# Optimization experiments

Measured on AMD Instinct MI355X. Metric: run time of the kernel, lower is better.

The kernel has to match this reference:

```python
import jax, jax.numpy as jnp
import numpy as np

B, DIM, H, W, NH, WS = 128, 768, 16, 16, 12, 16
N = H * W  # 256, equals window_size**2


def setup_inputs() -> dict:
    key = jax.random.key(0)
    ks = jax.random.split(key, 8)
    s = 0.02  # small init scale for params
    return {
        "x": jax.random.normal(ks[0], (B, DIM, H, W), dtype=jnp.float32),
        "face_priors": jax.random.uniform(ks[1], (B, N, N), dtype=jnp.float32),
        "qkv_w": jax.random.normal(ks[2], (3 * DIM, DIM), dtype=jnp.float32) * s,
        "qkv_b": jax.random.normal(ks[3], (3 * DIM,), dtype=jnp.float32) * s,
        "rel_table": jax.random.normal(ks[4], ((2 * WS - 1) * (2 * WS - 1), NH), dtype=jnp.float32) * s,
        "face_prior": jax.random.normal(ks[5], (1, NH, N, N), dtype=jnp.float32) * s,
        "proj_w": jax.random.normal(ks[6], (DIM, DIM), dtype=jnp.float32) * s,
        "proj_b": jax.random.normal(ks[7], (DIM,), dtype=jnp.float32) * s,
    }


def _relative_position_bias(rel_table, h, w):
    # Static index computation (h, w are Python ints under jit).
    coords = jnp.stack(jnp.meshgrid(jnp.arange(h), jnp.arange(w), indexing="ij"))  # [2,h,w]
    flat = coords.reshape(2, -1)                     # [2, N]
    rel = flat[:, :, None] - flat[:, None, :]        # [2, N, N]
    idx = (rel[0] + h - 1) * (2 * w - 1) + (rel[1] + w - 1)  # [N, N]
    return rel_table[idx].transpose(2, 0, 1)         # [nh, N, N]


def reference(x, face_priors, qkv_w, qkv_b, rel_table, face_prior, proj_w, proj_b):
    b, c, h, w = x.shape
    n = h * w
    nh = face_prior.shape[1]
    hd = c // nh
    scale = hd ** -0.5

    x_flat = x.reshape(b, c, n).transpose(0, 2, 1)   # [B, N, C]
    qkv = (x_flat @ qkv_w.T + qkv_b).reshape(b, n, 3, nh, hd).transpose(2, 0, 3, 1, 4)
    q, k, v = qkv[0], qkv[1], qkv[2]                 # each [B, nh, N, hd]

    attn = jnp.einsum("bhnd,bhmd->bhnm", q, k) * scale
    attn = attn + face_prior + _relative_position_bias(rel_table, h, w)[None]
    attn = attn * face_priors[:, None]               # broadcast over heads
    attn = jax.nn.softmax(attn, axis=-1)

    out = jnp.einsum("bhnm,bhmd->bhnd", attn, v)     # [B, nh, N, hd]
    out = out.transpose(0, 2, 1, 3).reshape(b, n, c)
    out = out @ proj_w.T + proj_b                    # [B, N, C]
    return out.transpose(0, 2, 1).reshape(b, c, h, w)
```

## Files before the change

### kernel.cpp

```cpp
#include <hip/hip_runtime.h>

#define B_   128
#define DIM_ 768
#define NH_  12
#define HD_  64
#define N_   256

using half8 = __attribute__((ext_vector_type(8))) _Float16;
using half4 = __attribute__((ext_vector_type(4))) _Float16;
using f32x4 = __attribute__((ext_vector_type(4))) float;
typedef unsigned short u16;
typedef unsigned int   u32;


#define GLDS16(srcp, dstp) \
    __builtin_amdgcn_global_load_lds( \
        (const __attribute__((address_space(1))) void*)(srcp), \
        (__attribute__((address_space(3))) void*)(dstp), 16, 0, 0)

__device__ __forceinline__ int xcd_chunked(int orig, int nwg) {
    int xcd = orig & 7, loc = orig >> 3;
    int qq = nwg >> 3, rr = nwg & 7;
    return (xcd < rr ? xcd * (qq + 1) : rr * (qq + 1) + (xcd - rr) * qq) + loc;
}

__global__ __launch_bounds__(256) void bias16_kernel(
    const float* __restrict__ face_prior, const float* __restrict__ rel_table,
    _Float16* __restrict__ b16)
{
    int gid = blockIdx.x * 256 + threadIdx.x;
    int idx = gid * 2;
    union { _Float16 s[2]; u32 u; } P;
    #pragma unroll
    for (int j = 0; j < 2; ++j) {
        int id = idx + j;
        int m = id & 255;
        int n = (id >> 8) & 255;
        int h = id >> 16;
        int rn = n >> 4, cn = n & 15;
        int rm = m >> 4, cm = m & 15;
        int ridx = (rn - rm + 15) * 31 + (cn - cm + 15);
        P.s[j] = (_Float16)(face_prior[id] + rel_table[ridx * NH_ + h]);
    }
    *(u32*)(b16 + idx) = P.u;
}

__global__ __launch_bounds__(256) void conv_f32_f16(
    const float* __restrict__ in, _Float16* __restrict__ o16, int n8)
{
    int i = blockIdx.x * 256 + threadIdx.x;
    if (i >= n8) return;
    float4 a = *(const float4*)(in + (size_t)i * 8);
    float4 b = *(const float4*)(in + (size_t)i * 8 + 4);
    float v[8] = {a.x, a.y, a.z, a.w, b.x, b.y, b.z, b.w};
    union { _Float16 s[8]; uint4 q; } H;
    #pragma unroll
    for (int j = 0; j < 8; ++j) H.s[j] = (_Float16)v[j];
    *(uint4*)(o16 + (size_t)i * 8) = H.q;
}

__global__ __launch_bounds__(256) void conv_w_f16_staged(
    const float* __restrict__ in, _Float16* __restrict__ o16, int nchunk)
{
    int gid = blockIdx.x * 256 + threadIdx.x;
    if (gid >= nchunk) return;
    int t   = gid / 12288;
    int rem = gid % 12288;
    int ks  = rem >> 9;
    int c   = rem & 511;
    int mtb = c >> 6, kgrp = (c >> 4) & 3, r16 = c & 15;
    int srow = t * 128 + mtb * 16 + r16;
    int sk   = ks * 32 + kgrp * 8;
    float4 a = *(const float4*)(in + (size_t)srow * DIM_ + sk);
    float4 b = *(const float4*)(in + (size_t)srow * DIM_ + sk + 4);
    float v[8] = {a.x, a.y, a.z, a.w, b.x, b.y, b.z, b.w};
    union { _Float16 s[8]; uint4 q; } H;
    #pragma unroll
    for (int j = 0; j < 8; ++j) H.s[j] = (_Float16)v[j];
    *(uint4*)(o16 + (size_t)gid * 8) = H.q;
}

__global__ __launch_bounds__(256) void conv_transpose_x_f16(
    const float* __restrict__ x, _Float16* __restrict__ xa)
{
    __shared__ float T[64][65];
    const int b = blockIdx.z, k0 = blockIdx.x * 64, n0 = blockIdx.y * 64;
    const int t = threadIdx.x;
    const float* xb = x + (size_t)b * DIM_ * N_;
    {
        int nn = t & 63, kg = t >> 6;
        #pragma unroll
        for (int r = 0; r < 16; ++r) {
            int kk = r * 4 + kg;
            T[kk][nn] = xb[(size_t)(k0 + kk) * N_ + n0 + nn];
        }
    }
    __syncthreads();
    {
        int kk2 = (t & 31) * 2, ng = t >> 5;
        #pragma unroll
        for (int r = 0; r < 8; ++r) {
            int nn = r * 8 + ng;
            union { _Float16 s[2]; u32 u; } P;
            P.s[0] = (_Float16)T[kk2][nn];
            P.s[1] = (_Float16)T[kk2 + 1][nn];
            int n = n0 + nn, k = k0 + kk2;
            int half = n >> 7, mtb = (n >> 4) & 7, r16 = n & 15;
            int ks = k >> 5, kgrp = (k >> 3) & 3, koff = k & 7;
            size_t o = ((((size_t)b * 2 + half) * 24 + ks) * 512
                        + mtb * 64 + kgrp * 16 + r16) * 8 + koff;
            *(u32*)(xa + o) = P.u;
        }
    }
}

__global__ __launch_bounds__(256) void qkv_gemm(
    const _Float16* __restrict__ w16, const _Float16* __restrict__ x16,
    const float* __restrict__ bvec,
    _Float16* __restrict__ q16, _Float16* __restrict__ k16,
    _Float16* __restrict__ v16,
    int b0, int cb)
{
    __shared__ __align__(16) _Float16 SW[4096], SX[4096];

    const int tid  = threadIdx.x;
    const int lane = tid & 63;
    const int wv   = tid >> 6;
    const int wr   = wv >> 1;
    const int wc   = wv & 1;

    const int wg = xcd_chunked(blockIdx.x, cb * 36);
    const int by = wg % 18;
    const int bx = wg / 18;
    const int bl = bx >> 1, half = bx & 1;
    const int b  = b0 + bl;

    const size_t wq0 = (size_t)by * 24 * 4096;
    const size_t xq0 = ((size_t)b * 2 + half) * 24 * 4096;

    f32x4 acc[4][4];
    #pragma unroll
    for (int i = 0; i < 4; ++i)
        #pragma unroll
        for (int j = 0; j < 4; ++j)
            acc[i][j] = (f32x4){0.f, 0.f, 0.f, 0.f};

    const int d0 = wv * 512;

    for (int ks = 0; ks < 24; ++ks) {
        const size_t wq = wq0 + (size_t)ks * 4096 + d0;
        const size_t xq = xq0 + (size_t)ks * 4096 + d0;
        #pragma unroll
        for (int s = 0; s < 2; ++s) {
            GLDS16(w16 + wq + s * 2048 + lane * 8, &SW[d0 + s * 2048]);
            GLDS16(x16 + xq + s * 2048 + lane * 8, &SX[d0 + s * 2048]);
        }
        __syncthreads();

        half8 ah[4];
        #pragma unroll
        for (int mt = 0; mt < 4; ++mt)
            ah[mt] = *(const half8*)&SW[((wr * 4 + mt) * 64 + lane) * 8];
        #pragma unroll
        for (int nt = 0; nt < 4; ++nt) {
            half8 bh = *(const half8*)&SX[((wc * 4 + nt) * 64 + lane) * 8];
            #pragma unroll
            for (int mt = 0; mt < 4; ++mt)
                acc[mt][nt] = __builtin_amdgcn_mfma_f32_16x16x32_f16(ah[mt], bh, acc[mt][nt], 0, 0, 0);
        }
        __syncthreads();
    }

    const int ocb = by * 128 + wr * 64 + (lane >> 4) * 4;
    const int nb  = half * 128 + wc * 64 + (lane & 15);

    #pragma unroll
    for (int mt = 0; mt < 4; ++mt) {
        int oc = ocb + mt * 16;
        float4 bv = *(const float4*)(bvec + oc);
        int which = oc / DIM_;
        int r = oc - which * DIM_;
        int hh = r >> 6, d = r & 63;
        _Float16* slab = (which == 0) ? q16 : (which == 1) ? k16 : v16;
        size_t rowbase = ((size_t)bl * NH_ + hh) * (N_ * HD_) + d;
        #pragma unroll
        for (int nt = 0; nt < 4; ++nt) {
            int n = nb + nt * 16;
            union { _Float16 s[4]; uint2 u; } H;
            H.s[0] = (_Float16)(acc[mt][nt][0] + bv.x);
            H.s[1] = (_Float16)(acc[mt][nt][1] + bv.y);
            H.s[2] = (_Float16)(acc[mt][nt][2] + bv.z);
            H.s[3] = (_Float16)(acc[mt][nt][3] + bv.w);
            *(uint2*)(slab + rowbase + (size_t)n * HD_) = H.u;
        }
    }
}

__global__ __launch_bounds__(256) void attn_mfma(
    const _Float16* __restrict__ q16, const _Float16* __restrict__ k16,
    const _Float16* __restrict__ v16,
    const _Float16* __restrict__ bias16, const _Float16* __restrict__ fpri16,
    _Float16* __restrict__ ao,
    int b0, int cb)
{
    extern __shared__ _Float16 ldsh[];
    _Float16* KL  = ldsh;
    _Float16* VtL = ldsh + 16384;
    const int tid  = threadIdx.x;
    const int lane = tid & 63;
    const int wv   = tid >> 6;
    _Float16* PL = ldsh + 32768 + wv * 512;

    const int bh = xcd_chunked(blockIdx.x, cb * NH_);
    const int bl = bh / NH_, h = bh % NH_;
    const int b  = b0 + bl;
    const size_t base = ((size_t)bl * NH_ + h) * (size_t)(N_ * HD_);

    const int l15 = lane & 15;
    const int lg  = lane >> 4;
    const int e   = (l15 & 3) << 1;

    #pragma unroll
    for (int s = 0; s < 8; ++s) {
        int idx = tid + s * 256;
        int r = idx >> 3, kc = (idx & 7) * 8;
        *(half8*)&KL[r * 64 + (kc ^ ((r & 7) << 3))] =
            *(const half8*)(k16 + base + (size_t)r * 64 + kc);
    }
    #pragma unroll
    for (int s = 0; s < 8; ++s) {
        int idx = tid + s * 256;
        int d = idx & 63, kkc = (idx >> 6) * 8;
        union { _Float16 sv[8]; half8 v; } t;
        #pragma unroll
        for (int j = 0; j < 8; ++j)
            t.sv[j] = v16[base + (size_t)(kkc + j) * 64 + d];
        *(half8*)&VtL[d * 256 + (kkc ^ ((d & 7) << 3))] = t.v;
    }
    __syncthreads();

    for (int qt = 0; qt < 4; ++qt) {
        const int qg = wv * 64 + qt * 16 + l15;
        const size_t qrow = base + (size_t)qg * 64;
        half8 bq[2];
        #pragma unroll
        for (int c = 0; c < 2; ++c)
            bq[c] = *(const half8*)(q16 + qrow + lg * 8 + c * 32);

        const _Float16* brow = bias16 + ((size_t)h * N_ + qg) * N_;
        const _Float16* frow = fpri16 + ((size_t)b * N_ + qg) * N_;

        float mrun = -1e30f, lrun = 0.f;
        f32x4 oacc[4];
        #pragma unroll
        for (int dt = 0; dt < 4; ++dt) oacc[dt] = (f32x4){0.f, 0.f, 0.f, 0.f};

        for (int ch = 0; ch < 2; ++ch) {
            f32x4 sacc[8];
            #pragma unroll
            for (int kt = 0; kt < 8; ++kt) {
                f32x4 sa = (f32x4){0.f, 0.f, 0.f, 0.f};
                int kr = ch * 128 + kt * 16 + l15;
                #pragma unroll
                for (int c = 0; c < 2; ++c) {
                    int kc = lg * 8 + c * 32;
                    half8 ah = *(const half8*)&KL[kr * 64 + (kc ^ ((kr & 7) << 3))];
                    sa = __builtin_amdgcn_mfma_f32_16x16x32_f16(ah, bq[c], sa, 0, 0, 0);
                }
                half4 bsv = *(const half4*)(brow + ch * 128 + kt * 16 + lg * 4);
                half4 fsv = *(const half4*)(frow + ch * 128 + kt * 16 + lg * 4);
                sacc[kt][0] = (sa[0] * 0.125f + (float)bsv[0]) * (float)fsv[0];
                sacc[kt][1] = (sa[1] * 0.125f + (float)bsv[1]) * (float)fsv[1];
                sacc[kt][2] = (sa[2] * 0.125f + (float)bsv[2]) * (float)fsv[2];
                sacc[kt][3] = (sa[3] * 0.125f + (float)bsv[3]) * (float)fsv[3];
            }

            float cmax = -1e30f;
            #pragma unroll
            for (int kt = 0; kt < 8; ++kt)
                cmax = fmaxf(cmax, fmaxf(fmaxf(sacc[kt][0], sacc[kt][1]),
                                         fmaxf(sacc[kt][2], sacc[kt][3])));
            cmax = fmaxf(cmax, __shfl_xor(cmax, 16));
            cmax = fmaxf(cmax, __shfl_xor(cmax, 32));
            float mnew = fmaxf(mrun, cmax);
            float corr = __expf(mrun - mnew);
            mrun = mnew;
            float csum = 0.f;
            #pragma unroll
            for (int kt = 0; kt < 8; ++kt) {
                #pragma unroll
                for (int j = 0; j < 4; ++j) {
                    float p = __expf(sacc[kt][j] - mnew);
                    sacc[kt][j] = p;
                    csum += p;
                }
            }
            csum += __shfl_xor(csum, 16);
            csum += __shfl_xor(csum, 32);
            lrun = lrun * corr + csum;
            #pragma unroll
            for (int dt = 0; dt < 4; ++dt) {
                oacc[dt][0] *= corr; oacc[dt][1] *= corr;
                oacc[dt][2] *= corr; oacc[dt][3] *= corr;
            }

            #pragma unroll
            for (int c2 = 0; c2 < 4; ++c2) {
                #pragma unroll
                for (int t = 0; t < 2; ++t) {
                    int kt = c2 * 2 + t;
                    union { _Float16 s[4]; uint2 u; } pw;
                    pw.s[0] = (_Float16)sacc[kt][0];
                    pw.s[1] = (_Float16)sacc[kt][1];
                    pw.s[2] = (_Float16)sacc[kt][2];
                    pw.s[3] = (_Float16)sacc[kt][3];
                    int u = (4 * t + lg) ^ e;
                    *(uint2*)&PL[l15 * 32 + u * 4] = pw.u;
                }
                half8 bp = *(const half8*)&PL[l15 * 32 + ((2 * lg) ^ e) * 4];
                int kc2 = ch * 128 + c2 * 32 + lg * 8;
                #pragma unroll
                for (int dt = 0; dt < 4; ++dt) {
                    int dr = dt * 16 + l15;
                    half8 av = *(const half8*)&VtL[dr * 256 + (kc2 ^ ((dr & 7) << 3))];
                    oacc[dt] = __builtin_amdgcn_mfma_f32_16x16x32_f16(av, bp, oacc[dt], 0, 0, 0);
                }
            }
        }

        float inv = 1.f / lrun;
        const int hf  = qg >> 7, mtb = (qg >> 4) & 7, r16 = qg & 15;
        #pragma unroll
        for (int dt = 0; dt < 4; ++dt) {
            int k = h * 64 + dt * 16 + lg * 4;
            int ks = k >> 5, kgrp = (k >> 3) & 3, koff = k & 7;
            size_t off = ((((size_t)(bl * 2 + hf) * 24 + ks) * 512)
                          + mtb * 64 + kgrp * 16 + r16) * 8 + koff;
            union { _Float16 s[4]; uint2 u; } H;
            #pragma unroll
            for (int j = 0; j < 4; ++j)
                H.s[j] = (_Float16)(oacc[dt][j] * inv);
            *(uint2*)(ao + off) = H.u;
        }
    }
}

__global__ __launch_bounds__(256) void proj_gemm(
    const _Float16* __restrict__ wst, const _Float16* __restrict__ ao,
    const float* __restrict__ bvec, float* __restrict__ outp,
    int b0, int cb)
{
    __shared__ __align__(16) _Float16 SW[4096], SX[4096];

    const int tid  = threadIdx.x;
    const int lane = tid & 63;
    const int wv   = tid >> 6;
    const int wr   = wv >> 1;
    const int wc   = wv & 1;

    const int wg = xcd_chunked(blockIdx.x, cb * 12);
    const int by = wg % 6;
    const int bx = wg / 6;
    const int bl = bx >> 1, half = bx & 1;
    const int b  = b0 + bl;

    const size_t wq0 = (size_t)by * 24 * 4096;
    const size_t xq0 = ((size_t)bl * 2 + half) * 24 * 4096;

    f32x4 acc[4][4];
    #pragma unroll
    for (int i = 0; i < 4; ++i)
        #pragma unroll
        for (int j = 0; j < 4; ++j)
            acc[i][j] = (f32x4){0.f, 0.f, 0.f, 0.f};

    const int d0 = wv * 512;

    for (int ks = 0; ks < 24; ++ks) {
        const size_t wq = wq0 + (size_t)ks * 4096 + d0;
        const size_t xq = xq0 + (size_t)ks * 4096 + d0;
        #pragma unroll
        for (int s = 0; s < 2; ++s) {
            GLDS16(wst + wq + s * 2048 + lane * 8, &SW[d0 + s * 2048]);
            GLDS16(ao  + xq + s * 2048 + lane * 8, &SX[d0 + s * 2048]);
        }
        __syncthreads();

        half8 ah[4];
        #pragma unroll
        for (int mt = 0; mt < 4; ++mt)
            ah[mt] = *(const half8*)&SW[((wr * 4 + mt) * 64 + lane) * 8];
        #pragma unroll
        for (int nt = 0; nt < 4; ++nt) {
            half8 bh = *(const half8*)&SX[((wc * 4 + nt) * 64 + lane) * 8];
            #pragma unroll
            for (int mt = 0; mt < 4; ++mt)
                acc[mt][nt] = __builtin_amdgcn_mfma_f32_16x16x32_f16(ah[mt], bh, acc[mt][nt], 0, 0, 0);
        }
        __syncthreads();
    }

    const int ocb = by * 128 + wr * 64 + (lane >> 4) * 4;
    const int nb  = half * 128 + wc * 64 + (lane & 15);

    #pragma unroll
    for (int mt = 0; mt < 4; ++mt) {
        int oc = ocb + mt * 16;
        float4 bv = *(const float4*)(bvec + oc);
        float* obase = outp + (size_t)b * DIM_ * N_ + (size_t)oc * N_;
        #pragma unroll
        for (int nt = 0; nt < 4; ++nt) {
            int n = nb + nt * 16;
            obase[0 * N_ + n] = acc[mt][nt][0] + bv.x;
            obase[1 * N_ + n] = acc[mt][nt][1] + bv.y;
            obase[2 * N_ + n] = acc[mt][nt][2] + bv.z;
            obase[3 * N_ + n] = acc[mt][nt][3] + bv.w;
        }
    }
}

extern "C" void kernel_launch(void* const* d_in, const int* in_sizes, int n_in,
                              void* d_out, int out_size, void* d_ws, size_t ws_size,
                              hipStream_t stream)
{
    const float* x           = (const float*)d_in[0];
    const float* face_priors = (const float*)d_in[1];
    const float* qkv_w       = (const float*)d_in[2];
    const float* qkv_b       = (const float*)d_in[3];
    const float* rel_table   = (const float*)d_in[4];
    const float* face_prior  = (const float*)d_in[5];
    const float* proj_w      = (const float*)d_in[6];
    const float* proj_b      = (const float*)d_in[7];
    float* out = (float*)d_out;

    _Float16* b16   = (_Float16*)d_ws;
    _Float16* fp16p = b16 + (size_t)NH_ * N_ * N_;
    _Float16* xa16  = fp16p + (size_t)B_ * N_ * N_;
    _Float16* qw16  = xa16 + (size_t)B_ * N_ * DIM_;
    _Float16* pw16  = qw16 + (size_t)3 * DIM_ * DIM_;
    _Float16* cbase = pw16 + (size_t)DIM_ * DIM_;

    const size_t PERSIST = 2ull * (NH_ * N_ * N_ + (size_t)B_ * N_ * N_
                         + (size_t)B_ * N_ * DIM_ + 4ull * DIM_ * DIM_);
    int CB = 1;
    const int cands[] = {128, 64, 32, 16, 8, 4, 2, 1};
    for (int ci = 0; ci < 8; ++ci) {
        if (PERSIST + (size_t)cands[ci] * 1572864ull <= ws_size) { CB = cands[ci]; break; }
    }
    const size_t SL = (size_t)CB * NH_ * N_ * HD_;
    _Float16* q16b = cbase;
    _Float16* k16b = q16b + SL;
    _Float16* v16b = k16b + SL;
    _Float16* aob  = v16b + SL;

    hipFuncSetAttribute((const void*)attn_mfma,
                        hipFuncAttributeMaxDynamicSharedMemorySize, 69632);

    bias16_kernel<<<(NH_ * N_ * N_ / 2) / 256, 256, 0, stream>>>(face_prior, rel_table, b16);
    conv_f32_f16<<<((B_ * N_ * N_ / 8) + 255) / 256, 256, 0, stream>>>(face_priors, fp16p, B_ * N_ * N_ / 8);
    conv_w_f16_staged<<<(18 * 12288 + 255) / 256, 256, 0, stream>>>(qkv_w, qw16, 18 * 12288);
    conv_w_f16_staged<<<(6 * 12288 + 255) / 256, 256, 0, stream>>>(proj_w, pw16, 6 * 12288);
    conv_transpose_x_f16<<<dim3(12, 4, B_), 256, 0, stream>>>(x, xa16);

    for (int b0 = 0; b0 < B_; b0 += CB) {
        qkv_gemm<<<CB * 36, 256, 0, stream>>>(
            qw16, xa16, qkv_b, q16b, k16b, v16b, b0, CB);

        attn_mfma<<<CB * NH_, 256, 69632, stream>>>(
            q16b, k16b, v16b, b16, fp16p, aob, b0, CB);

        proj_gemm<<<CB * 12, 256, 0, stream>>>(
            pw16, aob, proj_b, out, b0, CB);
    }
}
```

Baseline: 388.0 us.

## Enlarge QKV GEMM tiles to 256x256 with triple-buffered async LDS staging

The QKV projection GEMM moves from 128x128 tiles with 4 waves to 256x256 tiles with 8 waves per workgroup, so each wave accumulates 8x4 MFMA tiles. The weight and activation pre-staging kernels are re-laid out to match the larger tile format. The k-loop becomes a 3-stage global_load_lds pipeline with explicit vmcnt waits, replacing the synchronous load-then-compute loop. This aims to raise arithmetic intensity and hide memory latency, at the cost of 96KB of dynamic LDS per block, higher register pressure, and far fewer workgroups (CB*9) to fill the GPU.

```diff
diff --git a/kernel.cpp b/kernel.cpp
--- a/kernel.cpp
+++ b/kernel.cpp
@@ -11,7 +11,6 @@
 using f32x4 = __attribute__((ext_vector_type(4))) float;
 typedef unsigned short u16;
 typedef unsigned int   u32;
-
 
 #define GLDS16(srcp, dstp) \
     __builtin_amdgcn_global_load_lds( \
@@ -80,6 +79,27 @@
     *(uint4*)(o16 + (size_t)gid * 8) = H.q;
 }
 
+__global__ __launch_bounds__(256) void conv_qw_staged(
+    const float* __restrict__ in, _Float16* __restrict__ o16, int nchunk)
+{
+    int gid = blockIdx.x * 256 + threadIdx.x;
+    if (gid >= nchunk) return;
+    int t   = gid / 24576;
+    int rem = gid % 24576;
+    int ks  = rem >> 10;
+    int c   = rem & 1023;
+    int mtb = c >> 6, kg = (c >> 4) & 3, r16 = c & 15;
+    int srow = t * 256 + mtb * 16 + r16;
+    int sk   = ks * 32 + kg * 8;
+    float4 a = *(const float4*)(in + (size_t)srow * DIM_ + sk);
+    float4 b = *(const float4*)(in + (size_t)srow * DIM_ + sk + 4);
+    float v[8] = {a.x, a.y, a.z, a.w, b.x, b.y, b.z, b.w};
+    union { _Float16 s[8]; uint4 q; } H;
+    #pragma unroll
+    for (int j = 0; j < 8; ++j) H.s[j] = (_Float16)v[j];
+    *(uint4*)(o16 + (size_t)gid * 8) = H.q;
+}
+
 __global__ __launch_bounds__(256) void conv_transpose_x_f16(
     const float* __restrict__ x, _Float16* __restrict__ xa)
 {
@@ -105,84 +125,98 @@
             P.s[0] = (_Float16)T[kk2][nn];
             P.s[1] = (_Float16)T[kk2 + 1][nn];
             int n = n0 + nn, k = k0 + kk2;
-            int half = n >> 7, mtb = (n >> 4) & 7, r16 = n & 15;
-            int ks = k >> 5, kgrp = (k >> 3) & 3, koff = k & 7;
-            size_t o = ((((size_t)b * 2 + half) * 24 + ks) * 512
-                        + mtb * 64 + kgrp * 16 + r16) * 8 + koff;
+            int ks = k >> 5, kg = (k >> 3) & 3, koff = k & 7;
+            int mtb = n >> 4, r16 = n & 15;
+            size_t o = (((size_t)b * 24 + ks) * 1024
+                        + mtb * 64 + kg * 16 + r16) * 8 + koff;
             *(u32*)(xa + o) = P.u;
         }
     }
 }
 
-__global__ __launch_bounds__(256) void qkv_gemm(
+__global__ __launch_bounds__(512) void qkv_gemm(
     const _Float16* __restrict__ w16, const _Float16* __restrict__ x16,
     const float* __restrict__ bvec,
     _Float16* __restrict__ q16, _Float16* __restrict__ k16,
     _Float16* __restrict__ v16,
     int b0, int cb)
 {
-    __shared__ __align__(16) _Float16 SW[4096], SX[4096];
+    extern __shared__ _Float16 lds[];
 
     const int tid  = threadIdx.x;
     const int lane = tid & 63;
     const int wv   = tid >> 6;
-    const int wr   = wv >> 1;
-    const int wc   = wv & 1;
-
-    const int wg = xcd_chunked(blockIdx.x, cb * 36);
-    const int by = wg % 18;
-    const int bx = wg / 18;
-    const int bl = bx >> 1, half = bx & 1;
+    const int wr   = wv >> 2;
+    const int wc   = wv & 3;
+
+    const int wg = xcd_chunked(blockIdx.x, cb * 9);
+    const int by = wg % 9;
+    const int bl = wg / 9;
     const int b  = b0 + bl;
 
-    const size_t wq0 = (size_t)by * 24 * 4096;
-    const size_t xq0 = ((size_t)b * 2 + half) * 24 * 4096;
-
-    f32x4 acc[4][4];
-    #pragma unroll
-    for (int i = 0; i < 4; ++i)
+    const _Float16* wbase = w16 + (size_t)by * 24 * 8192;
+    const _Float16* xbase = x16 + (size_t)b  * 24 * 8192;
+
+    f32x4 acc[8][4];
+    #pragma unroll
+    for (int i = 0; i < 8; ++i)
         #pragma unroll
         for (int j = 0; j < 4; ++j)
             acc[i][j] = (f32x4){0.f, 0.f, 0.f, 0.f};
 
-    const int d0 = wv * 512;
-
-    for (int ks = 0; ks < 24; ++ks) {
-        const size_t wq = wq0 + (size_t)ks * 4096 + d0;
-        const size_t xq = xq0 + (size_t)ks * 4096 + d0;
-        #pragma unroll
-        for (int s = 0; s < 2; ++s) {
-            GLDS16(w16 + wq + s * 2048 + lane * 8, &SW[d0 + s * 2048]);
-            GLDS16(x16 + xq + s * 2048 + lane * 8, &SX[d0 + s * 2048]);
-        }
-        __syncthreads();
-
-        half8 ah[4];
-        #pragma unroll
-        for (int mt = 0; mt < 4; ++mt)
-            ah[mt] = *(const half8*)&SW[((wr * 4 + mt) * 64 + lane) * 8];
+    const int sbase = wv * 512;
+
+#define STAGE_T(tt, slot) do { \
+        const _Float16* ws_ = wbase + (size_t)(tt) * 8192; \
+        const _Float16* xs_ = xbase + (size_t)(tt) * 8192; \
+        _Float16* da_ = lds + (slot) * 8192; \
+        _Float16* db_ = lds + 24576 + (slot) * 8192; \
+        GLDS16(ws_ + sbase + lane * 8,        da_ + sbase); \
+        GLDS16(ws_ + 4096 + sbase + lane * 8, da_ + 4096 + sbase); \
+        GLDS16(xs_ + sbase + lane * 8,        db_ + sbase); \
+        GLDS16(xs_ + 4096 + sbase + lane * 8, db_ + 4096 + sbase); \
+    } while (0)
+
+    STAGE_T(0, 0); STAGE_T(1, 1); STAGE_T(2, 2);
+
+    int slot = 0;
+    for (int t = 0; t < 24; ++t) {
+        if (t < 22)       asm volatile("s_waitcnt vmcnt(8)" ::: "memory");
+        else if (t == 22) asm volatile("s_waitcnt vmcnt(4)" ::: "memory");
+        else              asm volatile("s_waitcnt vmcnt(0)" ::: "memory");
+        __builtin_amdgcn_s_barrier();
+
+        const _Float16* SAs = lds + slot * 8192;
+        const _Float16* SBs = lds + 24576 + slot * 8192;
+        half8 af[8];
+        #pragma unroll
+        for (int mt = 0; mt < 8; ++mt)
+            af[mt] = *(const half8*)&SAs[((wr * 8 + mt) * 64 + lane) * 8];
         #pragma unroll
         for (int nt = 0; nt < 4; ++nt) {
-            half8 bh = *(const half8*)&SX[((wc * 4 + nt) * 64 + lane) * 8];
-            #pragma unroll
-            for (int mt = 0; mt < 4; ++mt)
-                acc[mt][nt] = __builtin_amdgcn_mfma_f32_16x16x32_f16(ah[mt], bh, acc[mt][nt], 0, 0, 0);
-        }
-        __syncthreads();
-    }
-
-    const int ocb = by * 128 + wr * 64 + (lane >> 4) * 4;
-    const int nb  = half * 128 + wc * 64 + (lane & 15);
-
-    #pragma unroll
-    for (int mt = 0; mt < 4; ++mt) {
-        int oc = ocb + mt * 16;
-        float4 bv = *(const float4*)(bvec + oc);
-        int which = oc / DIM_;
-        int r = oc - which * DIM_;
-        int hh = r >> 6, d = r & 63;
-        _Float16* slab = (which == 0) ? q16 : (which == 1) ? k16 : v16;
-        size_t rowbase = ((size_t)bl * NH_ + hh) * (N_ * HD_) + d;
+            half8 bf = *(const half8*)&SBs[((wc * 4 + nt) * 64 + lane) * 8];
+            #pragma unroll
+            for (int mt = 0; mt < 8; ++mt)
+                acc[mt][nt] = __builtin_amdgcn_mfma_f32_16x16x32_f16(af[mt], bf, acc[mt][nt], 0, 0, 0);
+        }
+        __builtin_amdgcn_s_barrier();
+
+        if (t + 3 < 24) STAGE_T(t + 3, slot);
+        slot = (slot == 2) ? 0 : slot + 1;
+    }
+#undef STAGE_T
+
+    const int which = by / 3;
+    _Float16* slab = (which == 0) ? q16 : (which == 1) ? k16 : v16;
+    const int ocr0 = (by % 3) * 256 + wr * 128 + ((lane >> 4) << 2);
+    const int nb   = wc * 64 + (lane & 15);
+
+    #pragma unroll
+    for (int mt = 0; mt < 8; ++mt) {
+        int oc_in = ocr0 + mt * 16;
+        float4 bv = *(const float4*)(bvec + which * DIM_ + oc_in);
+        int hh = oc_in >> 6, d = oc_in & 63;
+        size_t rowbase = ((size_t)bl * NH_ + hh) * (size_t)(N_ * HD_) + d;
         #pragma unroll
         for (int nt = 0; nt < 4; ++nt) {
             int n = nb + nt * 16;
@@ -455,15 +489,17 @@
 
     hipFuncSetAttribute((const void*)attn_mfma,
                         hipFuncAttributeMaxDynamicSharedMemorySize, 69632);
+    hipFuncSetAttribute((const void*)qkv_gemm,
+                        hipFuncAttributeMaxDynamicSharedMemorySize, 98304);
 
     bias16_kernel<<<(NH_ * N_ * N_ / 2) / 256, 256, 0, stream>>>(face_prior, rel_table, b16);
     conv_f32_f16<<<((B_ * N_ * N_ / 8) + 255) / 256, 256, 0, stream>>>(face_priors, fp16p, B_ * N_ * N_ / 8);
-    conv_w_f16_staged<<<(18 * 12288 + 255) / 256, 256, 0, stream>>>(qkv_w, qw16, 18 * 12288);
+    conv_qw_staged<<<(9 * 24576 + 255) / 256, 256, 0, stream>>>(qkv_w, qw16, 9 * 24576);
     conv_w_f16_staged<<<(6 * 12288 + 255) / 256, 256, 0, stream>>>(proj_w, pw16, 6 * 12288);
     conv_transpose_x_f16<<<dim3(12, 4, B_), 256, 0, stream>>>(x, xa16);
 
     for (int b0 = 0; b0 < B_; b0 += CB) {
-        qkv_gemm<<<CB * 36, 256, 0, stream>>>(
+        qkv_gemm<<<CB * 9, 512, 98304, stream>>>(
             qw16, xa16, qkv_b, q16b, k16b, v16b, b0, CB);
 
         attn_mfma<<<CB * NH_, 256, 69632, stream>>>(
```

Result: no change. 387.9 us (-0.0%).
